# Optimization experiments

Measured on AMD Instinct MI355X. Metric: run time of the kernel, lower is better.

## Reference

```python
import jax, jax.numpy as jnp
import numpy as np
from jax import lax

B, T, V, E, H = 4096, 80, 10000, 100, 64


def setup_inputs() -> dict:
    key = jax.random.key(0)
    ks = jax.random.split(key, 8)
    return {
        "tokens": jax.random.randint(ks[0], (B, T), 0, V, dtype=jnp.int32),
        "emb": jax.random.normal(ks[1], (V, E), jnp.float32) * 0.05,
        "Wx0": jax.random.normal(ks[2], (E, H), jnp.float32) * (1.0 / np.sqrt(E)),
        "Wh0": jax.random.normal(ks[3], (H, H), jnp.float32) * (1.0 / np.sqrt(H)),
        "b0": jnp.zeros((H,), jnp.float32),
        "Wx1": jax.random.normal(ks[4], (H, H), jnp.float32) * (1.0 / np.sqrt(H)),
        "Wh1": jax.random.normal(ks[5], (H, H), jnp.float32) * (1.0 / np.sqrt(H)),
        "b1": jnp.zeros((H,), jnp.float32),
        "Wout": jax.random.normal(ks[6], (H, 1), jnp.float32) * (1.0 / np.sqrt(H)),
        "bout": jnp.zeros((1,), jnp.float32),
    }


def reference(tokens, emb, Wx0, Wh0, b0, Wx1, Wh1, b1, Wout, bout):
    # Embedding lookup: [B, T, E]
    x = emb[tokens]
    batch = x.shape[0]
    h0 = jnp.zeros((batch, Wh0.shape[0]), x.dtype)
    h1 = jnp.zeros((batch, Wh1.shape[0]), x.dtype)

    def step(carry, xt):
        h0, h1 = carry
        # SimpleRNNCell: h = tanh(x @ Wx + h_prev @ Wh + b)  (dropout off in eval)
        h0 = jnp.tanh(xt @ Wx0 + h0 @ Wh0 + b0)
        h1 = jnp.tanh(h0 @ Wx1 + h1 @ Wh1 + b1)
        return (h0, h1), None

    # scan over time: xs has shape [T, B, E]
    (h0, h1), _ = lax.scan(step, (h0, h1), jnp.swapaxes(x, 0, 1))
    logits = h1 @ Wout + bout  # [B, 1]
    return jax.nn.sigmoid(logits)
```

## Files before the change

kernel.cpp:

```cpp
#include <hip/hip_runtime.h>

#define BB 4096
#define TT 80
#define VV 10000
#define EE 100
#define HH 64
#define STR 68

typedef _Float16 f16x8 __attribute__((ext_vector_type(8)));
typedef _Float16 f16x4 __attribute__((ext_vector_type(4)));
typedef __attribute__((ext_vector_type(4))) float f4v;

#define MFMA(w, s, c) __builtin_amdgcn_mfma_f32_16x16x32_f16((w), (s), (c), 0, 0, 0)

#define BAR() do { asm volatile("s_waitcnt lgkmcnt(0)" ::: "memory"); \
                   __builtin_amdgcn_s_barrier();                      \
                   asm volatile("" ::: "memory"); } while (0)

__device__ __forceinline__ float fast_tanh(float x) {
    float e = __builtin_amdgcn_exp2f(x * 2.8853900817779268f);
    return 1.0f - 2.0f * __builtin_amdgcn_rcpf(e + 1.0f);
}

__device__ __forceinline__ f16x8 load_wfrag_hi(const float* __restrict__ W, int kf,
                                               int g, int c) {
    union { _Float16 h[8]; f16x8 v; } th;
#pragma unroll
    for (int i = 0; i < 8; ++i)
        th.h[i] = (_Float16)W[(32 * kf + 8 * g + i) * HH + c];
    return th.v;
}

__global__ __launch_bounds__(256) void emb2_kernel(const float* __restrict__ emb,
                                                   const float* __restrict__ Wx0,
                                                   const float* __restrict__ b0,
                                                   _Float16* __restrict__ emb2h) {
    const int tid = threadIdx.x;
    const int wid = tid >> 6;
    const int l = tid & 63;
    const int g = l >> 4;
    const int r16 = l & 15;
    const int c = 16 * wid + r16;
    const int jcol = 16 * wid + 4 * g;
    const int vr = blockIdx.x * 16 + r16;

    f16x8 wa[4];
#pragma unroll
    for (int kf = 0; kf < 4; ++kf) {
        union { _Float16 h[8]; f16x8 v; } t;
#pragma unroll
        for (int i = 0; i < 8; ++i) {
            int e = 32 * kf + 8 * g + i;
            t.h[i] = (e < EE) ? (_Float16)Wx0[e * HH + c] : (_Float16)0.f;
        }
        wa[kf] = t.v;
    }
    const float* er = emb + (size_t)vr * EE;
    f4v acc = *(const f4v*)&b0[jcol];
#pragma unroll
    for (int kf = 0; kf < 4; ++kf) {
        union { _Float16 h[8]; f16x8 v; } tb;
#pragma unroll
        for (int i = 0; i < 8; ++i) {
            int e = 32 * kf + 8 * g + i;
            tb.h[i] = (e < EE) ? (_Float16)er[e] : (_Float16)0.f;
        }
        acc = MFMA(wa[kf], tb.v, acc);
    }
    f16x4 o;
#pragma unroll
    for (int q = 0; q < 4; ++q) o[q] = (_Float16)acc[q];
    *(f16x4*)&emb2h[(size_t)vr * HH + jcol] = o;
}

__global__ __launch_bounds__(512, 1) void rnn_pipe(
    const int* __restrict__ tokens, const _Float16* __restrict__ emb2,
    const float* __restrict__ Wh0, const float* __restrict__ Wx1,
    const float* __restrict__ Wh1, const float* __restrict__ b1,
    const float* __restrict__ Wout, const float* __restrict__ bout,
    float* __restrict__ out) {
    __shared__ __align__(16) _Float16 H0[2][16][STR];
    __shared__ __align__(16) _Float16 H1[2][16][STR];
    __shared__ __align__(16) int tokT[TT][16];
    __shared__ float Pred[4][16];

    const int tid = threadIdx.x;
    const int w8 = tid >> 6;
    const int l = tid & 63;
    const int g = l >> 4;
    const int r16 = l & 15;
    const bool isL0 = (w8 < 4);
    const int tile = isL0 ? w8 : (w8 - 4);
    const int c = 16 * tile + r16;
    const int jcol = 16 * tile + 4 * g;
    const int R = blockIdx.x * 16;

    for (int i = tid; i < 16 * TT; i += 512) {
        int r = i / TT, t = i - r * TT;
        tokT[t][r] = tokens[R * TT + i] << 7;
    }

    f16x8 wA[2], wB[2];
    if (isL0) {
        wA[0] = load_wfrag_hi(Wh0, 0, g, c);
        wA[1] = load_wfrag_hi(Wh0, 1, g, c);
        wB[0] = wB[1] = (f16x8)0;
    } else {
        wA[0] = load_wfrag_hi(Wx1, 0, g, c);
        wA[1] = load_wfrag_hi(Wx1, 1, g, c);
        wB[0] = load_wfrag_hi(Wh1, 0, g, c);
        wB[1] = load_wfrag_hi(Wh1, 1, g, c);
    }
    const f4v b1v = *(const f4v*)&b1[jcol];
    const f4v wov = *(const f4v*)&Wout[jcol];
    const f4v z4 = {0.f, 0.f, 0.f, 0.f};
    const char* ebase = (const char*)emb2 + (size_t)jcol * 2;

    BAR();

    f16x8 a0[2] = {(f16x8)0, (f16x8)0};
    f16x8 a1[2] = {(f16x8)0, (f16x8)0};

    f16x4 xc = (f16x4)0, xn = (f16x4)0;
    if (isL0) {
        xc = *(const f16x4*)(ebase + tokT[0][r16]);
        xn = *(const f16x4*)(ebase + tokT[1][r16]);
        f16x4 ph;
#pragma unroll
        for (int q = 0; q < 4; ++q) ph[q] = (_Float16)fast_tanh((float)xc[q]);
        *(f16x4*)&H0[0][r16][jcol] = ph;
        xc = xn;
    }
    BAR();
    a0[0] = *(const f16x8*)&H0[0][r16][8 * g];
    a0[1] = *(const f16x8*)&H0[0][r16][32 + 8 * g];

#pragma unroll 2
    for (int p = 1; p <= TT - 1; ++p) {
        const int par = p & 1;
        if (isL0) {
            int pn = (p + 1 <= TT - 1) ? p + 1 : TT - 1;
            xn = *(const f16x4*)(ebase + tokT[pn][r16]);
            f4v A1 = {(float)xc[0], (float)xc[1], (float)xc[2], (float)xc[3]};
            A1 = MFMA(wA[0], a0[0], A1);
            A1 = MFMA(wA[1], a0[1], A1);
            f16x4 p0;
#pragma unroll
            for (int q = 0; q < 4; ++q) p0[q] = (_Float16)fast_tanh(A1[q]);
            *(f16x4*)&H0[par][r16][jcol] = p0;
            xc = xn;
        } else {
            f4v C1 = b1v;
            C1 = MFMA(wA[0], a0[0], C1);
            C1 = MFMA(wA[1], a0[1], C1);
            f4v C3 = MFMA(wB[0], a1[0], z4);
            C3 = MFMA(wB[1], a1[1], C3);
            f4v acc1 = C1 + C3;
            f16x4 p1;
#pragma unroll
            for (int q = 0; q < 4; ++q) p1[q] = (_Float16)fast_tanh(acc1[q]);
            *(f16x4*)&H1[par][r16][jcol] = p1;
        }
        BAR();
        a0[0] = *(const f16x8*)&H0[par][r16][8 * g];
        a0[1] = *(const f16x8*)&H0[par][r16][32 + 8 * g];
        if (!isL0) {
            a1[0] = *(const f16x8*)&H1[par][r16][8 * g];
            a1[1] = *(const f16x8*)&H1[par][r16][32 + 8 * g];
        }
    }

    if (!isL0) {
        f4v C1 = b1v;
        C1 = MFMA(wA[0], a0[0], C1);
        C1 = MFMA(wA[1], a0[1], C1);
        f4v C3 = MFMA(wB[0], a1[0], z4);
        C3 = MFMA(wB[1], a1[1], C3);
        f4v acc1 = C1 + C3;
        float pp = fast_tanh(acc1[0]) * wov[0];
        pp = fmaf(fast_tanh(acc1[1]), wov[1], pp);
        pp = fmaf(fast_tanh(acc1[2]), wov[2], pp);
        pp = fmaf(fast_tanh(acc1[3]), wov[3], pp);
        pp += __shfl_xor(pp, 16, 64);
        pp += __shfl_xor(pp, 32, 64);
        if (l < 16) Pred[tile][l] = pp;
    }
    BAR();
    if (tid < 16) {
        float logit = Pred[0][tid] + Pred[1][tid] + Pred[2][tid] +
                      Pred[3][tid] + bout[0];
        out[R + tid] = __builtin_amdgcn_rcpf(
            1.0f + __builtin_amdgcn_exp2f(-1.4426950408889634f * logit));
    }
}

extern "C" void kernel_launch(void* const* d_in, const int* in_sizes, int n_in,
                              void* d_out, int out_size, void* d_ws, size_t ws_size,
                              hipStream_t stream) {
    const int*   tokens = (const int*)  d_in[0];
    const float* emb    = (const float*)d_in[1];
    const float* Wx0    = (const float*)d_in[2];
    const float* Wh0    = (const float*)d_in[3];
    const float* b0     = (const float*)d_in[4];
    const float* Wx1    = (const float*)d_in[5];
    const float* Wh1    = (const float*)d_in[6];
    const float* b1     = (const float*)d_in[7];
    const float* Wout   = (const float*)d_in[8];
    const float* bout   = (const float*)d_in[9];
    float* out  = (float*)d_out;
    _Float16* emb2h = (_Float16*)d_ws;

    emb2_kernel<<<VV / 16, 256, 0, stream>>>(emb, Wx0, b0, emb2h);
    rnn_pipe<<<BB / 16, 512, 0, stream>>>(tokens, emb2h, Wh0, Wx1, Wh1, b1,
                                          Wout, bout, out);
}
```

Before: 38.14 us.

## Run full two-layer recurrence in one wave with register-resident hidden state

The eight-wave block that passed hidden states through LDS with a barrier every step is replaced by a single 64-lane wave per 16-row batch tile. That wave computes all four column tiles of both layers. The weight fragments are loaded with a permuted K ordering, so each MFMA output layout directly forms the next step's B-operand fragment in registers, which removes the LDS round trips and barriers. In exchange, each step's work is serialized within one wave (24 dependent-ish MFMAs per step) and register pressure rises, and only 256 single-wave blocks occupy the GPU.

```diff
diff --git a/kernel.cpp b/kernel.cpp
--- a/kernel.cpp
+++ b/kernel.cpp
@@ -5,7 +5,6 @@
 #define VV 10000
 #define EE 100
 #define HH 64
-#define STR 68
 
 typedef _Float16 f16x8 __attribute__((ext_vector_type(8)));
 typedef _Float16 f16x4 __attribute__((ext_vector_type(4)));
@@ -13,21 +12,19 @@
 
 #define MFMA(w, s, c) __builtin_amdgcn_mfma_f32_16x16x32_f16((w), (s), (c), 0, 0, 0)
 
-#define BAR() do { asm volatile("s_waitcnt lgkmcnt(0)" ::: "memory"); \
-                   __builtin_amdgcn_s_barrier();                      \
-                   asm volatile("" ::: "memory"); } while (0)
-
 __device__ __forceinline__ float fast_tanh(float x) {
     float e = __builtin_amdgcn_exp2f(x * 2.8853900817779268f);
     return 1.0f - 2.0f * __builtin_amdgcn_rcpf(e + 1.0f);
 }
 
-__device__ __forceinline__ f16x8 load_wfrag_hi(const float* __restrict__ W, int kf,
-                                               int g, int c) {
+__device__ __forceinline__ f16x8 load_wfrag_pi_hi(const float* __restrict__ W,
+                                                  int kf, int g, int c) {
     union { _Float16 h[8]; f16x8 v; } th;
 #pragma unroll
-    for (int i = 0; i < 8; ++i)
-        th.h[i] = (_Float16)W[(32 * kf + 8 * g + i) * HH + c];
+    for (int i = 0; i < 8; ++i) {
+        int k = 16 * (i >> 1) + 4 * g + 2 * kf + (i & 1);
+        th.h[i] = (_Float16)W[k * HH + c];
+    }
     return th.v;
 }
 
@@ -73,123 +70,112 @@
     *(f16x4*)&emb2h[(size_t)vr * HH + jcol] = o;
 }
 
-__global__ __launch_bounds__(512, 1) void rnn_pipe(
+__global__ __launch_bounds__(64, 1) void rnn_chain(
     const int* __restrict__ tokens, const _Float16* __restrict__ emb2,
     const float* __restrict__ Wh0, const float* __restrict__ Wx1,
     const float* __restrict__ Wh1, const float* __restrict__ b1,
     const float* __restrict__ Wout, const float* __restrict__ bout,
     float* __restrict__ out) {
-    __shared__ __align__(16) _Float16 H0[2][16][STR];
-    __shared__ __align__(16) _Float16 H1[2][16][STR];
-    __shared__ __align__(16) int tokT[TT][16];
-    __shared__ float Pred[4][16];
-
-    const int tid = threadIdx.x;
-    const int w8 = tid >> 6;
-    const int l = tid & 63;
+    __shared__ int tokB[TT][16];
+
+    const int l = threadIdx.x;
     const int g = l >> 4;
     const int r16 = l & 15;
-    const bool isL0 = (w8 < 4);
-    const int tile = isL0 ? w8 : (w8 - 4);
-    const int c = 16 * tile + r16;
-    const int jcol = 16 * tile + 4 * g;
     const int R = blockIdx.x * 16;
 
-    for (int i = tid; i < 16 * TT; i += 512) {
+    for (int i = l; i < 16 * TT; i += 64) {
         int r = i / TT, t = i - r * TT;
-        tokT[t][r] = tokens[R * TT + i] << 7;
-    }
-
-    f16x8 wA[2], wB[2];
-    if (isL0) {
-        wA[0] = load_wfrag_hi(Wh0, 0, g, c);
-        wA[1] = load_wfrag_hi(Wh0, 1, g, c);
-        wB[0] = wB[1] = (f16x8)0;
-    } else {
-        wA[0] = load_wfrag_hi(Wx1, 0, g, c);
-        wA[1] = load_wfrag_hi(Wx1, 1, g, c);
-        wB[0] = load_wfrag_hi(Wh1, 0, g, c);
-        wB[1] = load_wfrag_hi(Wh1, 1, g, c);
-    }
-    const f4v b1v = *(const f4v*)&b1[jcol];
-    const f4v wov = *(const f4v*)&Wout[jcol];
+        tokB[t][r] = tokens[R * TT + i] << 7;
+    }
+
+    f16x8 w0[4][2], wx[4][2], w1[4][2];
+    f4v b1v[4];
+#pragma unroll
+    for (int t = 0; t < 4; ++t) {
+        int c = 16 * t + r16;
+        w0[t][0] = load_wfrag_pi_hi(Wh0, 0, g, c);
+        w0[t][1] = load_wfrag_pi_hi(Wh0, 1, g, c);
+        wx[t][0] = load_wfrag_pi_hi(Wx1, 0, g, c);
+        wx[t][1] = load_wfrag_pi_hi(Wx1, 1, g, c);
+        w1[t][0] = load_wfrag_pi_hi(Wh1, 0, g, c);
+        w1[t][1] = load_wfrag_pi_hi(Wh1, 1, g, c);
+        b1v[t] = *(const f4v*)&b1[16 * t + 4 * g];
+    }
     const f4v z4 = {0.f, 0.f, 0.f, 0.f};
-    const char* ebase = (const char*)emb2 + (size_t)jcol * 2;
-
-    BAR();
-
-    f16x8 a0[2] = {(f16x8)0, (f16x8)0};
-    f16x8 a1[2] = {(f16x8)0, (f16x8)0};
-
-    f16x4 xc = (f16x4)0, xn = (f16x4)0;
-    if (isL0) {
-        xc = *(const f16x4*)(ebase + tokT[0][r16]);
-        xn = *(const f16x4*)(ebase + tokT[1][r16]);
-        f16x4 ph;
-#pragma unroll
-        for (int q = 0; q < 4; ++q) ph[q] = (_Float16)fast_tanh((float)xc[q]);
-        *(f16x4*)&H0[0][r16][jcol] = ph;
-        xc = xn;
-    }
-    BAR();
-    a0[0] = *(const f16x8*)&H0[0][r16][8 * g];
-    a0[1] = *(const f16x8*)&H0[0][r16][32 + 8 * g];
-
-#pragma unroll 2
-    for (int p = 1; p <= TT - 1; ++p) {
-        const int par = p & 1;
-        if (isL0) {
-            int pn = (p + 1 <= TT - 1) ? p + 1 : TT - 1;
-            xn = *(const f16x4*)(ebase + tokT[pn][r16]);
-            f4v A1 = {(float)xc[0], (float)xc[1], (float)xc[2], (float)xc[3]};
-            A1 = MFMA(wA[0], a0[0], A1);
-            A1 = MFMA(wA[1], a0[1], A1);
-            f16x4 p0;
-#pragma unroll
-            for (int q = 0; q < 4; ++q) p0[q] = (_Float16)fast_tanh(A1[q]);
-            *(f16x4*)&H0[par][r16][jcol] = p0;
-            xc = xn;
-        } else {
-            f4v C1 = b1v;
-            C1 = MFMA(wA[0], a0[0], C1);
-            C1 = MFMA(wA[1], a0[1], C1);
-            f4v C3 = MFMA(wB[0], a1[0], z4);
-            C3 = MFMA(wB[1], a1[1], C3);
-            f4v acc1 = C1 + C3;
-            f16x4 p1;
-#pragma unroll
-            for (int q = 0; q < 4; ++q) p1[q] = (_Float16)fast_tanh(acc1[q]);
-            *(f16x4*)&H1[par][r16][jcol] = p1;
-        }
-        BAR();
-        a0[0] = *(const f16x8*)&H0[par][r16][8 * g];
-        a0[1] = *(const f16x8*)&H0[par][r16][32 + 8 * g];
-        if (!isL0) {
-            a1[0] = *(const f16x8*)&H1[par][r16][8 * g];
-            a1[1] = *(const f16x8*)&H1[par][r16][32 + 8 * g];
-        }
-    }
-
-    if (!isL0) {
-        f4v C1 = b1v;
-        C1 = MFMA(wA[0], a0[0], C1);
-        C1 = MFMA(wA[1], a0[1], C1);
-        f4v C3 = MFMA(wB[0], a1[0], z4);
-        C3 = MFMA(wB[1], a1[1], C3);
-        f4v acc1 = C1 + C3;
-        float pp = fast_tanh(acc1[0]) * wov[0];
-        pp = fmaf(fast_tanh(acc1[1]), wov[1], pp);
-        pp = fmaf(fast_tanh(acc1[2]), wov[2], pp);
-        pp = fmaf(fast_tanh(acc1[3]), wov[3], pp);
-        pp += __shfl_xor(pp, 16, 64);
-        pp += __shfl_xor(pp, 32, 64);
-        if (l < 16) Pred[tile][l] = pp;
-    }
-    BAR();
-    if (tid < 16) {
-        float logit = Pred[0][tid] + Pred[1][tid] + Pred[2][tid] +
-                      Pred[3][tid] + bout[0];
-        out[R + tid] = __builtin_amdgcn_rcpf(
+    const char* eb = (const char*)emb2 + (size_t)(4 * g) * 2;
+
+    f16x8 f0h = (f16x8)0, f1h = (f16x8)0;
+    f16x8 f0g = (f16x8)0, f1g = (f16x8)0;
+    f4v vv[4];
+
+    f16x4 xcs[4], xns[4];
+    {
+        int tb = tokB[0][r16];
+#pragma unroll
+        for (int t = 0; t < 4; ++t)
+            xcs[t] = *(const f16x4*)(eb + tb + 32 * t);
+    }
+
+#pragma unroll 1
+    for (int p = 0; p < TT; ++p) {
+        int pn = (p + 1 < TT) ? p + 1 : TT - 1;
+        int tbn = tokB[pn][r16];
+#pragma unroll
+        for (int t = 0; t < 4; ++t)
+            xns[t] = *(const f16x4*)(eb + tbn + 32 * t);
+
+        union PK { _Float16 h[8]; f16x8 v; } p0, p1;
+#pragma unroll
+        for (int t = 0; t < 4; ++t) {
+            f4v a = {(float)xcs[t][0], (float)xcs[t][1],
+                     (float)xcs[t][2], (float)xcs[t][3]};
+            a = MFMA(w0[t][0], f0h, a);
+            a = MFMA(w0[t][1], f1h, a);
+            p0.h[2 * t]     = (_Float16)fast_tanh(a[0]);
+            p0.h[2 * t + 1] = (_Float16)fast_tanh(a[1]);
+            p1.h[2 * t]     = (_Float16)fast_tanh(a[2]);
+            p1.h[2 * t + 1] = (_Float16)fast_tanh(a[3]);
+        }
+        f0h = p0.v; f1h = p1.v;
+
+        union PK q0, q1;
+#pragma unroll
+        for (int t = 0; t < 4; ++t) {
+            f4v a = b1v[t];
+            a = MFMA(wx[t][0], f0h, a);
+            a = MFMA(wx[t][1], f1h, a);
+            f4v b = MFMA(w1[t][0], f0g, z4);
+            b = MFMA(w1[t][1], f1g, b);
+            f4v s = a + b;
+            vv[t][0] = fast_tanh(s[0]);
+            vv[t][1] = fast_tanh(s[1]);
+            vv[t][2] = fast_tanh(s[2]);
+            vv[t][3] = fast_tanh(s[3]);
+            q0.h[2 * t]     = (_Float16)vv[t][0];
+            q0.h[2 * t + 1] = (_Float16)vv[t][1];
+            q1.h[2 * t]     = (_Float16)vv[t][2];
+            q1.h[2 * t + 1] = (_Float16)vv[t][3];
+        }
+        f0g = q0.v; f1g = q1.v;
+
+#pragma unroll
+        for (int t = 0; t < 4; ++t) xcs[t] = xns[t];
+    }
+
+    float pp = 0.f;
+#pragma unroll
+    for (int t = 0; t < 4; ++t) {
+        f4v wov = *(const f4v*)&Wout[16 * t + 4 * g];
+        pp = fmaf(vv[t][0], wov[0], pp);
+        pp = fmaf(vv[t][1], wov[1], pp);
+        pp = fmaf(vv[t][2], wov[2], pp);
+        pp = fmaf(vv[t][3], wov[3], pp);
+    }
+    pp += __shfl_xor(pp, 16, 64);
+    pp += __shfl_xor(pp, 32, 64);
+    if (l < 16) {
+        float logit = pp + bout[0];
+        out[R + l] = __builtin_amdgcn_rcpf(
             1.0f + __builtin_amdgcn_exp2f(-1.4426950408889634f * logit));
     }
 }
@@ -211,6 +197,6 @@
     _Float16* emb2h = (_Float16*)d_ws;
 
     emb2_kernel<<<VV / 16, 256, 0, stream>>>(emb, Wx0, b0, emb2h);
-    rnn_pipe<<<BB / 16, 512, 0, stream>>>(tokens, emb2h, Wh0, Wx1, Wh1, b1,
+    rnn_chain<<<BB / 16, 64, 0, stream>>>(tokens, emb2h, Wh0, Wx1, Wh1, b1,
                                           Wout, bout, out);
 }
```

Measured after the change: 73.49 us. +92.7%, slower.
